# Kernel optimization log

Hardware: AMD Instinct MI355X
Metric: run time of the kernel (lower is better)

The kernel has to match this reference:

```python
import jax, jax.numpy as jnp
import numpy as np

B, S, D, E, K, FF = 4, 2048, 1024, 8, 2, 4096  # batch, seq, d_model, experts, top-k, 4*d_model


def setup_inputs() -> dict:
    key = jax.random.key(0)
    k0, k1, k2, k3 = jax.random.split(key, 4)
    scale = 0.02
    return {
        "x": jax.random.normal(k0, (B, S, D), jnp.float32),
        "gate_w": jax.random.normal(k1, (D, E), jnp.float32) * scale,
        "w1": jax.random.normal(k2, (E, D, FF), jnp.float32) * scale,
        "b1": jnp.zeros((E, FF), jnp.float32),
        "w2": jax.random.normal(k3, (E, FF, D), jnp.float32) * scale,
        "b2": jnp.zeros((E, D), jnp.float32),
    }


def reference(x, gate_w, w1, b1, w2, b2):
    # Gating: top-k logits, softmax over the selected k (matches torch.topk + softmax)
    logits = jnp.einsum("bsd,de->bse", x, gate_w)  # [B,S,E]
    vals, idxs = jax.lax.top_k(logits, K)           # [B,S,K]
    w = jax.nn.softmax(vals, axis=-1)               # [B,S,K]
    n_exp = gate_w.shape[-1]
    # Per-token combine weight for each expert (0 if not selected)
    combine = jnp.sum(jax.nn.one_hot(idxs, n_exp, dtype=x.dtype) * w[..., None], axis=-2)  # [B,S,E]

    out = jnp.zeros_like(x)
    for e in range(n_exp):  # fixed small loop over experts
        h = jax.nn.silu(jnp.einsum("bsd,df->bsf", x, w1[e]) + b1[e])  # dropout = identity (eval)
        y = jnp.einsum("bsf,fd->bsd", h, w2[e]) + b2[e]
        out = out + combine[..., e:e + 1] * y
    return out
```

## Files before the change

### kernel.cpp

```cpp
#include <hip/hip_runtime.h>
#include <math.h>

#define Tt 8192
#define Dd 1024
#define Ee 8
#define FFf 4096
#define SLOTS (Tt*2)

typedef unsigned short u16;
typedef unsigned int u32;
typedef __attribute__((ext_vector_type(8))) __bf16 bf16x8;
typedef __attribute__((ext_vector_type(4))) float f32x4;

__device__ __forceinline__ u16 f2bf(float f) {
  union { float f; u32 u; } v; v.f = f;
  u32 u = v.u;
  return (u16)((u + 0x7FFFu + ((u >> 16) & 1u)) >> 16);
}
__device__ __forceinline__ float bf2f(u16 h) {
  union { u32 u; float f; } v; v.u = ((u32)h) << 16; return v.f;
}
__device__ __forceinline__ void gl2lds16(const u16* g, u16* l) {
  __builtin_amdgcn_global_load_lds((const __attribute__((address_space(1))) void*)g,
                                   (__attribute__((address_space(3))) void*)l, 16, 0, 0);
}

__global__ void gate_topk_kernel(const float* __restrict__ x,
                                 const float* __restrict__ gw,
                                 int* __restrict__ counts,
                                 int* __restrict__ tok_e,
                                 float* __restrict__ tok_w,
                                 u16* __restrict__ xb) {
  int wave = (int)((blockIdx.x * blockDim.x + threadIdx.x) >> 6);
  int lane = threadIdx.x & 63;
  if (wave >= Tt) return;
  const float* xrow = x + (size_t)wave * Dd;
  float p[Ee];
#pragma unroll
  for (int e = 0; e < Ee; e++) p[e] = 0.f;
  int d0 = lane * 16;
  float xv[16];
#pragma unroll
  for (int i = 0; i < 16; i++) {
    xv[i] = xrow[d0 + i];
    const float* g = gw + (size_t)(d0 + i) * Ee;
#pragma unroll
    for (int e = 0; e < Ee; e++) p[e] += xv[i] * g[e];
  }
  {
    uint4 o0, o1;
    o0.x = (u32)f2bf(xv[0]) | ((u32)f2bf(xv[1]) << 16);
    o0.y = (u32)f2bf(xv[2]) | ((u32)f2bf(xv[3]) << 16);
    o0.z = (u32)f2bf(xv[4]) | ((u32)f2bf(xv[5]) << 16);
    o0.w = (u32)f2bf(xv[6]) | ((u32)f2bf(xv[7]) << 16);
    o1.x = (u32)f2bf(xv[8]) | ((u32)f2bf(xv[9]) << 16);
    o1.y = (u32)f2bf(xv[10]) | ((u32)f2bf(xv[11]) << 16);
    o1.z = (u32)f2bf(xv[12]) | ((u32)f2bf(xv[13]) << 16);
    o1.w = (u32)f2bf(xv[14]) | ((u32)f2bf(xv[15]) << 16);
    u16* dp = xb + (size_t)wave * Dd + d0;
    *(uint4*)dp = o0;
    *(uint4*)(dp + 8) = o1;
  }
#pragma unroll
  for (int e = 0; e < Ee; e++) {
    for (int off = 32; off > 0; off >>= 1) p[e] += __shfl_xor(p[e], off, 64);
  }
  if (lane == 0) {
    int e0 = 0; float v0 = p[0];
#pragma unroll
    for (int e = 1; e < Ee; e++) if (p[e] > v0) { v0 = p[e]; e0 = e; }
    int e1 = -1; float v1 = -INFINITY;
#pragma unroll
    for (int e = 0; e < Ee; e++) if (e != e0 && p[e] > v1) { v1 = p[e]; e1 = e; }
    float w0 = 1.f / (1.f + expf(v1 - v0));
    float w1 = 1.f - w0;
    tok_e[wave * 2 + 0] = e0; tok_e[wave * 2 + 1] = e1;
    tok_w[wave * 2 + 0] = w0; tok_w[wave * 2 + 1] = w1;
    atomicAdd(&counts[e0], 1);
    atomicAdd(&counts[e1], 1);
  }
}

__global__ __launch_bounds__(256) void wconv_kernel(const float* __restrict__ src,
                                                    u16* __restrict__ dst, int R, int C) {
  __shared__ float t[64][65];
  int e = blockIdx.z;
  size_t ebase = (size_t)e * R * C;
  int r0 = blockIdx.y * 64, c0 = blockIdx.x * 64;
  int tid = threadIdx.x;
  int row = tid >> 2, q = tid & 3;
  const float* sp = src + ebase + (size_t)(r0 + row) * C + c0 + q * 16;
  f32x4 v0 = *(const f32x4*)(sp);
  f32x4 v1 = *(const f32x4*)(sp + 4);
  f32x4 v2 = *(const f32x4*)(sp + 8);
  f32x4 v3 = *(const f32x4*)(sp + 12);
#pragma unroll
  for (int k = 0; k < 4; k++) t[row][q * 16 + k] = v0[k];
#pragma unroll
  for (int k = 0; k < 4; k++) t[row][q * 16 + 4 + k] = v1[k];
#pragma unroll
  for (int k = 0; k < 4; k++) t[row][q * 16 + 8 + k] = v2[k];
#pragma unroll
  for (int k = 0; k < 4; k++) t[row][q * 16 + 12 + k] = v3[k];
  __syncthreads();
  float c[16];
#pragma unroll
  for (int k = 0; k < 16; k++) c[k] = t[q * 16 + k][row];
  uint4 d0, d1;
  d0.x = (u32)f2bf(c[0]) | ((u32)f2bf(c[1]) << 16);
  d0.y = (u32)f2bf(c[2]) | ((u32)f2bf(c[3]) << 16);
  d0.z = (u32)f2bf(c[4]) | ((u32)f2bf(c[5]) << 16);
  d0.w = (u32)f2bf(c[6]) | ((u32)f2bf(c[7]) << 16);
  d1.x = (u32)f2bf(c[8]) | ((u32)f2bf(c[9]) << 16);
  d1.y = (u32)f2bf(c[10]) | ((u32)f2bf(c[11]) << 16);
  d1.z = (u32)f2bf(c[12]) | ((u32)f2bf(c[13]) << 16);
  d1.w = (u32)f2bf(c[14]) | ((u32)f2bf(c[15]) << 16);
  u16* dp = dst + ebase + (size_t)(c0 + row) * R + r0 + q * 16;
  *(uint4*)dp = d0;
  *(uint4*)(dp + 8) = d1;
}

__global__ void scan_kernel(const int* __restrict__ counts,
                            int* __restrict__ offsets, int* __restrict__ cursors) {
  if (threadIdx.x == 0 && blockIdx.x == 0) {
    int acc = 0;
    for (int e = 0; e < Ee; e++) { offsets[e] = acc; cursors[e] = acc; acc += counts[e]; }
  }
}

__global__ void scatter_kernel(const int* __restrict__ tok_e, const float* __restrict__ tok_w,
                               int* __restrict__ cursors,
                               int* __restrict__ slot_token, float* __restrict__ slot_w,
                               int* __restrict__ tok_slot) {
  int t = blockIdx.x * blockDim.x + threadIdx.x;
  if (t >= Tt) return;
#pragma unroll
  for (int k = 0; k < 2; k++) {
    int e = tok_e[t * 2 + k];
    int pos = atomicAdd(&cursors[e], 1);
    slot_token[pos] = t;
    slot_w[pos] = tok_w[t * 2 + k];
    tok_slot[t * 2 + k] = pos;
  }
}

#define MFMA16R                                                                   \
  do {                                                                            \
    acc[0][0] = __builtin_amdgcn_mfma_f32_16x16x32_bf16(a0, b0, acc[0][0], 0, 0, 0); \
    acc[0][1] = __builtin_amdgcn_mfma_f32_16x16x32_bf16(a0, b1, acc[0][1], 0, 0, 0); \
    acc[0][2] = __builtin_amdgcn_mfma_f32_16x16x32_bf16(a0, b2, acc[0][2], 0, 0, 0); \
    acc[0][3] = __builtin_amdgcn_mfma_f32_16x16x32_bf16(a0, b3, acc[0][3], 0, 0, 0); \
    acc[1][0] = __builtin_amdgcn_mfma_f32_16x16x32_bf16(a1, b0, acc[1][0], 0, 0, 0); \
    acc[1][1] = __builtin_amdgcn_mfma_f32_16x16x32_bf16(a1, b1, acc[1][1], 0, 0, 0); \
    acc[1][2] = __builtin_amdgcn_mfma_f32_16x16x32_bf16(a1, b2, acc[1][2], 0, 0, 0); \
    acc[1][3] = __builtin_amdgcn_mfma_f32_16x16x32_bf16(a1, b3, acc[1][3], 0, 0, 0); \
    acc[2][0] = __builtin_amdgcn_mfma_f32_16x16x32_bf16(a2, b0, acc[2][0], 0, 0, 0); \
    acc[2][1] = __builtin_amdgcn_mfma_f32_16x16x32_bf16(a2, b1, acc[2][1], 0, 0, 0); \
    acc[2][2] = __builtin_amdgcn_mfma_f32_16x16x32_bf16(a2, b2, acc[2][2], 0, 0, 0); \
    acc[2][3] = __builtin_amdgcn_mfma_f32_16x16x32_bf16(a2, b3, acc[2][3], 0, 0, 0); \
    acc[3][0] = __builtin_amdgcn_mfma_f32_16x16x32_bf16(a3, b0, acc[3][0], 0, 0, 0); \
    acc[3][1] = __builtin_amdgcn_mfma_f32_16x16x32_bf16(a3, b1, acc[3][1], 0, 0, 0); \
    acc[3][2] = __builtin_amdgcn_mfma_f32_16x16x32_bf16(a3, b2, acc[3][2], 0, 0, 0); \
    acc[3][3] = __builtin_amdgcn_mfma_f32_16x16x32_bf16(a3, b3, acc[3][3], 0, 0, 0); \
  } while (0)

template<int KDIM, int NDIM, int EPI, int GATHER>
__global__ __launch_bounds__(512, 2) void moe_gemm_r(
    const u16* __restrict__ A, const u16* __restrict__ BT,
    const float* __restrict__ bias,
    const int* __restrict__ offsets, const int* __restrict__ counts,
    const int* __restrict__ slot_token, const float* __restrict__ slot_w,
    u16* __restrict__ O16, float* __restrict__ Of) {
  constexpr int NT = KDIM / 64;
  int e = blockIdx.z;
  int cnt = counts[e];
  int rb = blockIdx.y;
  if (rb * 128 >= cnt) return;
  int off = offsets[e];
  int n0 = blockIdx.x * 256;

  __shared__ u16 S[49152];

  int tid = threadIdx.x;
  int lane = tid & 63, wave = tid >> 6;
  int wr = wave >> 2, wc = wave & 3;
  int lr = lane & 15, g = lane >> 4;

  const u16* BTe = BT + (size_t)e * NDIM * KDIM;

  const u16* aSrc[2];
  const u16* bSrc[4];
  int amax = off + cnt - 1;
#pragma unroll
  for (int s = 0; s < 2; s++) {
    int c = tid + s * 512;
    int lc = c ^ (((c >> 5) & 1) << 1);
    int rl = (lc >> 2) & 127, seg = lc & 3;
    int slotRow = off + rb * 128 + rl;
    if (slotRow > amax) slotRow = amax;
    int arow = GATHER ? slot_token[slotRow] : slotRow;
    aSrc[s] = A + (size_t)arow * KDIM + s * 32 + seg * 8;
  }
#pragma unroll
  for (int s = 0; s < 4; s++) {
    int c = tid + s * 512;
    int lc = c ^ (((c >> 5) & 1) << 1);
    int row = (lc >> 2) & 255, seg = lc & 3;
    int ks = s >> 1;
    bSrc[s] = BTe + (size_t)(n0 + row) * KDIM + ks * 32 + seg * 8;
  }

  auto stA = [&](int u, int ks) {
    gl2lds16(aSrc[ks] + (size_t)u * 64, &S[(u & 1) * 8192 + ks * 4096 + wave * 512]);
  };
  auto stB = [&](int u, int ks) {
    u16* base = &S[16384 + (u & 1) * 16384 + ks * 8192 + wave * 512];
    gl2lds16(bSrc[ks * 2] + (size_t)u * 64, base);
    gl2lds16(bSrc[ks * 2 + 1] + (size_t)u * 64, base + 4096);
  };
  auto rdA = [&](int dbuf, int ks, int i) -> bf16x8 {
    int rl = wr * 64 + i * 16 + lr;
    int logb = rl * 64 + g * 16;
    int phys = logb ^ (((rl >> 3) & 1) << 5);
    return *reinterpret_cast<const bf16x8*>(&S[dbuf * 8192 + ks * 4096 + (phys >> 1)]);
  };
  auto rdB = [&](int dbuf, int ks, int j) -> bf16x8 {
    int row = wc * 64 + j * 16 + lr;
    int logb = row * 64 + g * 16;
    int phys = logb ^ (((row >> 3) & 1) << 5);
    return *reinterpret_cast<const bf16x8*>(&S[16384 + dbuf * 16384 + ks * 8192 + (phys >> 1)]);
  };

  f32x4 acc[4][4];
#pragma unroll
  for (int i = 0; i < 4; i++)
#pragma unroll
    for (int j = 0; j < 4; j++) acc[i][j] = (f32x4)(0.0f);

  stB(0, 0); stA(0, 0);
  stB(0, 1); stA(0, 1);
  stB(1, 0); stA(1, 0);
  asm volatile("s_waitcnt vmcnt(3)" ::: "memory");
  __builtin_amdgcn_s_barrier();

  for (int t = 0; t < NT; ++t) {
    int dbuf = t & 1;
    {
      bf16x8 a0 = rdA(dbuf, 0, 0), a1 = rdA(dbuf, 0, 1),
             a2 = rdA(dbuf, 0, 2), a3 = rdA(dbuf, 0, 3);
      bf16x8 b0 = rdB(dbuf, 0, 0), b1 = rdB(dbuf, 0, 1),
             b2 = rdB(dbuf, 0, 2), b3 = rdB(dbuf, 0, 3);
      if (t + 1 < NT) { stB(t + 1, 1); stA(t + 1, 1); }
      __builtin_amdgcn_s_barrier();
      asm volatile("s_waitcnt lgkmcnt(0)" ::: "memory");
      __builtin_amdgcn_sched_barrier(0);
      __builtin_amdgcn_s_setprio(1);
      MFMA16R;
      __builtin_amdgcn_s_setprio(0);
      __builtin_amdgcn_s_barrier();
    }
    {
      bf16x8 a0 = rdA(dbuf, 1, 0), a1 = rdA(dbuf, 1, 1),
             a2 = rdA(dbuf, 1, 2), a3 = rdA(dbuf, 1, 3);
      bf16x8 b0 = rdB(dbuf, 1, 0), b1 = rdB(dbuf, 1, 1),
             b2 = rdB(dbuf, 1, 2), b3 = rdB(dbuf, 1, 3);
      if (t + 2 < NT) {
        stB(t + 2, 0); stA(t + 2, 0);
        asm volatile("s_waitcnt vmcnt(3)" ::: "memory");
      } else if (t + 1 < NT) {
        asm volatile("s_waitcnt vmcnt(0)" ::: "memory");
      }
      __builtin_amdgcn_s_barrier();
      asm volatile("s_waitcnt lgkmcnt(0)" ::: "memory");
      __builtin_amdgcn_sched_barrier(0);
      __builtin_amdgcn_s_setprio(1);
      MFMA16R;
      __builtin_amdgcn_s_setprio(0);
      __builtin_amdgcn_s_barrier();
    }
  }

  int rlim = cnt - rb * 128;
#pragma unroll
  for (int i = 0; i < 4; i++)
#pragma unroll
    for (int q = 0; q < 4; q++) {
      int m = wr * 64 + i * 16 + g * 4 + q;
      if (m < rlim) {
        int slot = off + rb * 128 + m;
#pragma unroll
        for (int j = 0; j < 4; j++) {
          int n = n0 + wc * 64 + j * 16 + lr;
          float v = acc[i][j][q] + bias[e * NDIM + n];
          if (EPI == 0) {
            float sv = v / (1.f + expf(-v));
            O16[(size_t)slot * NDIM + n] = f2bf(sv);
          } else if (EPI == 1) {
            O16[(size_t)slot * NDIM + n] = f2bf(v * slot_w[slot]);
          } else {
            atomicAdd(Of + (size_t)slot_token[slot] * NDIM + n, v * slot_w[slot]);
          }
        }
      }
    }
}

__global__ void combine_kernel(const u16* __restrict__ y, const int* __restrict__ tok_slot,
                               float* __restrict__ out) {
  int gid = blockIdx.x * blockDim.x + threadIdx.x;
  int t = gid >> 7;
  int seg = gid & 127;
  int s0 = tok_slot[t * 2 + 0], s1 = tok_slot[t * 2 + 1];
  uint4 a = *(const uint4*)(y + (size_t)s0 * Dd + seg * 8);
  uint4 b = *(const uint4*)(y + (size_t)s1 * Dd + seg * 8);
  f32x4 o0, o1;
  o0[0] = bf2f((u16)a.x) + bf2f((u16)b.x);
  o0[1] = bf2f((u16)(a.x >> 16)) + bf2f((u16)(b.x >> 16));
  o0[2] = bf2f((u16)a.y) + bf2f((u16)b.y);
  o0[3] = bf2f((u16)(a.y >> 16)) + bf2f((u16)(b.y >> 16));
  o1[0] = bf2f((u16)a.z) + bf2f((u16)b.z);
  o1[1] = bf2f((u16)(a.z >> 16)) + bf2f((u16)(b.z >> 16));
  o1[2] = bf2f((u16)a.w) + bf2f((u16)b.w);
  o1[3] = bf2f((u16)(a.w >> 16)) + bf2f((u16)(b.w >> 16));
  float* op = out + (size_t)t * Dd + seg * 8;
  *(f32x4*)op = o0;
  *(f32x4*)(op + 4) = o1;
}

extern "C" void kernel_launch(void* const* d_in, const int* in_sizes, int n_in,
                              void* d_out, int out_size, void* d_ws, size_t ws_size,
                              hipStream_t stream) {
  const float* x  = (const float*)d_in[0];
  const float* gw = (const float*)d_in[1];
  const float* w1 = (const float*)d_in[2];
  const float* b1 = (const float*)d_in[3];
  const float* w2 = (const float*)d_in[4];
  const float* b2 = (const float*)d_in[5];
  float* out = (float*)d_out;

  char* ws = (char*)d_ws;
  size_t off_counts = 0;
  size_t off_offsets = 256;
  size_t off_cursors = 512;
  size_t off_tok_e = 1024;
  size_t off_tok_w     = off_tok_e + (size_t)Tt * 2 * 4;
  size_t off_tok_slot  = off_tok_w + (size_t)Tt * 2 * 4;
  size_t off_slot_token= off_tok_slot + (size_t)Tt * 2 * 4;
  size_t off_slot_w    = off_slot_token + (size_t)SLOTS * 4;
  size_t off_xb        = off_slot_w + (size_t)SLOTS * 4;
  size_t off_h         = off_xb + (size_t)Tt * Dd * 2;
  size_t off_wT        = off_h + (size_t)SLOTS * FFf * 2;
  size_t off_y         = off_wT + (size_t)Ee * Dd * FFf * 2;
  size_t need_atomic   = off_y;
  size_t need_full     = off_y + (size_t)SLOTS * Dd * 2;
  if (ws_size < need_atomic) return;
  int use_combine = (ws_size >= need_full) ? 1 : 0;

  int* counts     = (int*)(ws + off_counts);
  int* offsets    = (int*)(ws + off_offsets);
  int* cursors    = (int*)(ws + off_cursors);
  int* tok_e      = (int*)(ws + off_tok_e);
  float* tok_w    = (float*)(ws + off_tok_w);
  int* tok_slot   = (int*)(ws + off_tok_slot);
  int* slot_token = (int*)(ws + off_slot_token);
  float* slot_w   = (float*)(ws + off_slot_w);
  u16* xb         = (u16*)(ws + off_xb);
  u16* h          = (u16*)(ws + off_h);
  u16* wT         = (u16*)(ws + off_wT);
  u16* y          = (u16*)(ws + off_y);

  hipMemsetAsync(ws, 0, 1024, stream);

  gate_topk_kernel<<<Tt / 4, 256, 0, stream>>>(x, gw, counts, tok_e, tok_w, xb);
  scan_kernel<<<1, 64, 0, stream>>>(counts, offsets, cursors);
  scatter_kernel<<<Tt / 256, 256, 0, stream>>>(tok_e, tok_w, cursors, slot_token, slot_w, tok_slot);

  {
    dim3 gc(FFf / 64, Dd / 64, Ee);
    wconv_kernel<<<gc, 256, 0, stream>>>(w1, wT, Dd, FFf);
  }
  {
    dim3 g1(FFf / 256, 64, Ee);
    moe_gemm_r<Dd, FFf, 0, 1><<<g1, 512, 0, stream>>>(xb, wT, b1, offsets, counts,
                                                      slot_token, slot_w, h, nullptr);
  }
  {
    dim3 gc(Dd / 64, FFf / 64, Ee);
    wconv_kernel<<<gc, 256, 0, stream>>>(w2, wT, FFf, Dd);
  }
  if (use_combine) {
    dim3 g2(Dd / 256, 64, Ee);
    moe_gemm_r<FFf, Dd, 1, 0><<<g2, 512, 0, stream>>>(h, wT, b2, offsets, counts,
                                                      slot_token, slot_w, y, nullptr);
    combine_kernel<<<(Tt * 128) / 256, 256, 0, stream>>>(y, tok_slot, out);
  } else {
    hipMemsetAsync(d_out, 0, (size_t)out_size * sizeof(float), stream);
    dim3 g2(Dd / 256, 64, Ee);
    moe_gemm_r<FFf, Dd, 2, 0><<<g2, 512, 0, stream>>>(h, wT, b2, offsets, counts,
                                                      slot_token, slot_w, nullptr, out);
  }
}
```

Before: 823.2 us.

## Triple-buffer LDS tiles in MoE GEMM to deepen the prefetch pipeline

Changes the expert GEMM's shared-memory staging from double to triple buffering, so loads for K-tile t+2 and t+3 are issued while tile t is computed. The vmcnt waits are retuned to match. LDS grows from 96KB to 144KB per block, which with 512 threads and 2 blocks per CU may reduce occupancy. The kernel is also wrapped in per-variant __global__ entry points, and the grid y-dimension is written as Tt/128, which equals the previous 64.

```diff
diff --git a/kernel.cpp b/kernel.cpp
--- a/kernel.cpp
+++ b/kernel.cpp
@@ -165,7 +165,7 @@
   } while (0)
 
 template<int KDIM, int NDIM, int EPI, int GATHER>
-__global__ __launch_bounds__(512, 2) void moe_gemm_r(
+__device__ __forceinline__ void moe_body(
     const u16* __restrict__ A, const u16* __restrict__ BT,
     const float* __restrict__ bias,
     const int* __restrict__ offsets, const int* __restrict__ counts,
@@ -179,7 +179,7 @@
   int off = offsets[e];
   int n0 = blockIdx.x * 256;
 
-  __shared__ u16 S[49152];
+  __shared__ u16 S[73728];
 
   int tid = threadIdx.x;
   int lane = tid & 63, wave = tid >> 6;
@@ -210,25 +210,25 @@
     bSrc[s] = BTe + (size_t)(n0 + row) * KDIM + ks * 32 + seg * 8;
   }
 
-  auto stA = [&](int u, int ks) {
-    gl2lds16(aSrc[ks] + (size_t)u * 64, &S[(u & 1) * 8192 + ks * 4096 + wave * 512]);
+  auto stA = [&](int b, int u, int ks) {
+    gl2lds16(aSrc[ks] + (size_t)u * 64, &S[b * 8192 + ks * 4096 + wave * 512]);
   };
-  auto stB = [&](int u, int ks) {
-    u16* base = &S[16384 + (u & 1) * 16384 + ks * 8192 + wave * 512];
+  auto stB = [&](int b, int u, int ks) {
+    u16* base = &S[24576 + b * 16384 + ks * 8192 + wave * 512];
     gl2lds16(bSrc[ks * 2] + (size_t)u * 64, base);
     gl2lds16(bSrc[ks * 2 + 1] + (size_t)u * 64, base + 4096);
   };
-  auto rdA = [&](int dbuf, int ks, int i) -> bf16x8 {
+  auto rdA = [&](int b, int ks, int i) -> bf16x8 {
     int rl = wr * 64 + i * 16 + lr;
     int logb = rl * 64 + g * 16;
     int phys = logb ^ (((rl >> 3) & 1) << 5);
-    return *reinterpret_cast<const bf16x8*>(&S[dbuf * 8192 + ks * 4096 + (phys >> 1)]);
+    return *reinterpret_cast<const bf16x8*>(&S[b * 8192 + ks * 4096 + (phys >> 1)]);
   };
-  auto rdB = [&](int dbuf, int ks, int j) -> bf16x8 {
+  auto rdB = [&](int b, int ks, int j) -> bf16x8 {
     int row = wc * 64 + j * 16 + lr;
     int logb = row * 64 + g * 16;
     int phys = logb ^ (((row >> 3) & 1) << 5);
-    return *reinterpret_cast<const bf16x8*>(&S[16384 + dbuf * 16384 + ks * 8192 + (phys >> 1)]);
+    return *reinterpret_cast<const bf16x8*>(&S[24576 + b * 16384 + ks * 8192 + (phys >> 1)]);
   };
 
   f32x4 acc[4][4];
@@ -237,20 +237,28 @@
 #pragma unroll
     for (int j = 0; j < 4; j++) acc[i][j] = (f32x4)(0.0f);
 
-  stB(0, 0); stA(0, 0);
-  stB(0, 1); stA(0, 1);
-  stB(1, 0); stA(1, 0);
-  asm volatile("s_waitcnt vmcnt(3)" ::: "memory");
+  stB(0, 0, 0); stA(0, 0, 0);
+  stB(0, 0, 1); stA(0, 0, 1);
+  stB(1, 1, 0); stA(1, 1, 0);
+  stB(1, 1, 1); stA(1, 1, 1);
+  stB(2, 2, 0); stA(2, 2, 0);
+  asm volatile("s_waitcnt vmcnt(9)" ::: "memory");
   __builtin_amdgcn_s_barrier();
 
+  int cur = 0;
   for (int t = 0; t < NT; ++t) {
-    int dbuf = t & 1;
+    int n2 = cur + 2; if (n2 >= 3) n2 -= 3;
     {
-      bf16x8 a0 = rdA(dbuf, 0, 0), a1 = rdA(dbuf, 0, 1),
-             a2 = rdA(dbuf, 0, 2), a3 = rdA(dbuf, 0, 3);
-      bf16x8 b0 = rdB(dbuf, 0, 0), b1 = rdB(dbuf, 0, 1),
-             b2 = rdB(dbuf, 0, 2), b3 = rdB(dbuf, 0, 3);
-      if (t + 1 < NT) { stB(t + 1, 1); stA(t + 1, 1); }
+      bf16x8 a0 = rdA(cur, 0, 0), a1 = rdA(cur, 0, 1),
+             a2 = rdA(cur, 0, 2), a3 = rdA(cur, 0, 3);
+      bf16x8 b0 = rdB(cur, 0, 0), b1 = rdB(cur, 0, 1),
+             b2 = rdB(cur, 0, 2), b3 = rdB(cur, 0, 3);
+      if (t + 2 < NT) {
+        stB(n2, t + 2, 1); stA(n2, t + 2, 1);
+        asm volatile("s_waitcnt vmcnt(9)" ::: "memory");
+      } else if (t + 1 < NT) {
+        asm volatile("s_waitcnt vmcnt(3)" ::: "memory");
+      }
       __builtin_amdgcn_s_barrier();
       asm volatile("s_waitcnt lgkmcnt(0)" ::: "memory");
       __builtin_amdgcn_sched_barrier(0);
@@ -260,13 +268,13 @@
       __builtin_amdgcn_s_barrier();
     }
     {
-      bf16x8 a0 = rdA(dbuf, 1, 0), a1 = rdA(dbuf, 1, 1),
-             a2 = rdA(dbuf, 1, 2), a3 = rdA(dbuf, 1, 3);
-      bf16x8 b0 = rdB(dbuf, 1, 0), b1 = rdB(dbuf, 1, 1),
-             b2 = rdB(dbuf, 1, 2), b3 = rdB(dbuf, 1, 3);
-      if (t + 2 < NT) {
-        stB(t + 2, 0); stA(t + 2, 0);
-        asm volatile("s_waitcnt vmcnt(3)" ::: "memory");
+      bf16x8 a0 = rdA(cur, 1, 0), a1 = rdA(cur, 1, 1),
+             a2 = rdA(cur, 1, 2), a3 = rdA(cur, 1, 3);
+      bf16x8 b0 = rdB(cur, 1, 0), b1 = rdB(cur, 1, 1),
+             b2 = rdB(cur, 1, 2), b3 = rdB(cur, 1, 3);
+      if (t + 3 < NT) {
+        stB(cur, t + 3, 0); stA(cur, t + 3, 0);
+        asm volatile("s_waitcnt vmcnt(9)" ::: "memory");
       } else if (t + 1 < NT) {
         asm volatile("s_waitcnt vmcnt(0)" ::: "memory");
       }
@@ -278,6 +286,7 @@
       __builtin_amdgcn_s_setprio(0);
       __builtin_amdgcn_s_barrier();
     }
+    cur = cur + 1; if (cur >= 3) cur -= 3;
   }
 
   int rlim = cnt - rb * 128;
@@ -303,6 +312,28 @@
         }
       }
     }
+}
+
+__global__ __launch_bounds__(512, 2) void moe_g1_kernel(
+    const u16* __restrict__ A, const u16* __restrict__ BT, const float* __restrict__ bias,
+    const int* __restrict__ offsets, const int* __restrict__ counts,
+    const int* __restrict__ slot_token, const float* __restrict__ slot_w,
+    u16* __restrict__ O16) {
+  moe_body<Dd, FFf, 0, 1>(A, BT, bias, offsets, counts, slot_token, slot_w, O16, nullptr);
+}
+__global__ __launch_bounds__(512, 2) void moe_g2_kernel(
+    const u16* __restrict__ A, const u16* __restrict__ BT, const float* __restrict__ bias,
+    const int* __restrict__ offsets, const int* __restrict__ counts,
+    const int* __restrict__ slot_token, const float* __restrict__ slot_w,
+    u16* __restrict__ O16) {
+  moe_body<FFf, Dd, 1, 0>(A, BT, bias, offsets, counts, slot_token, slot_w, O16, nullptr);
+}
+__global__ __launch_bounds__(512, 2) void moe_g2_atomic_kernel(
+    const u16* __restrict__ A, const u16* __restrict__ BT, const float* __restrict__ bias,
+    const int* __restrict__ offsets, const int* __restrict__ counts,
+    const int* __restrict__ slot_token, const float* __restrict__ slot_w,
+    float* __restrict__ Of) {
+  moe_body<FFf, Dd, 2, 0>(A, BT, bias, offsets, counts, slot_token, slot_w, nullptr, Of);
 }
 
 __global__ void combine_kernel(const u16* __restrict__ y, const int* __restrict__ tok_slot,
@@ -380,23 +411,23 @@
     wconv_kernel<<<gc, 256, 0, stream>>>(w1, wT, Dd, FFf);
   }
   {
-    dim3 g1(FFf / 256, 64, Ee);
-    moe_gemm_r<Dd, FFf, 0, 1><<<g1, 512, 0, stream>>>(xb, wT, b1, offsets, counts,
-                                                      slot_token, slot_w, h, nullptr);
+    dim3 g1(FFf / 256, Tt / 128, Ee);
+    moe_g1_kernel<<<g1, 512, 0, stream>>>(xb, wT, b1, offsets, counts,
+                                          slot_token, slot_w, h);
   }
   {
     dim3 gc(Dd / 64, FFf / 64, Ee);
     wconv_kernel<<<gc, 256, 0, stream>>>(w2, wT, FFf, Dd);
   }
   if (use_combine) {
-    dim3 g2(Dd / 256, 64, Ee);
-    moe_gemm_r<FFf, Dd, 1, 0><<<g2, 512, 0, stream>>>(h, wT, b2, offsets, counts,
-                                                      slot_token, slot_w, y, nullptr);
+    dim3 g2(Dd / 256, Tt / 128, Ee);
+    moe_g2_kernel<<<g2, 512, 0, stream>>>(h, wT, b2, offsets, counts,
+                                          slot_token, slot_w, y);
     combine_kernel<<<(Tt * 128) / 256, 256, 0, stream>>>(y, tok_slot, out);
   } else {
     hipMemsetAsync(d_out, 0, (size_t)out_size * sizeof(float), stream);
-    dim3 g2(Dd / 256, 64, Ee);
-    moe_gemm_r<FFf, Dd, 2, 0><<<g2, 512, 0, stream>>>(h, wT, b2, offsets, counts,
-                                                      slot_token, slot_w, nullptr, out);
-  }
-}
+    dim3 g2(Dd / 256, Tt / 128, Ee);
+    moe_g2_atomic_kernel<<<g2, 512, 0, stream>>>(h, wT, b2, offsets, counts,
+                                                 slot_token, slot_w, out);
+  }
+}
```

Result: no change. 827.7 us (+0.5%).
